# Optimization experiments

Measured on AMD Instinct MI355X. Metric: run time of the kernel, lower is better.

The kernel has to match this reference:

```python
import jax, jax.numpy as jnp
import numpy as np

B, T, C, H, E, K = 4, 2048, 512, 2048, 8, 2


def setup_inputs() -> dict:
    key = jax.random.key(0)
    ks = jax.random.split(key, 7)
    s_r = 1.0 / np.sqrt(C)
    s_h = 1.0 / np.sqrt(H)
    return {
        "x": jax.random.normal(ks[0], (B, T, C), dtype=jnp.float32),
        "Wr": jax.random.uniform(ks[1], (C, E), jnp.float32, -s_r, s_r),
        "br": jax.random.uniform(ks[2], (E,), jnp.float32, -s_r, s_r),
        "W1": jax.random.uniform(ks[3], (E, C, H), jnp.float32, -s_r, s_r),
        "b1": jax.random.uniform(ks[4], (E, H), jnp.float32, -s_r, s_r),
        "W2": jax.random.uniform(ks[5], (E, H, C), jnp.float32, -s_h, s_h),
        "b2": jax.random.uniform(ks[6], (E, C), jnp.float32, -s_h, s_h),
    }


def reference(x, Wr, br, W1, b1, W2, b2):
    # Router logits [B,T,E]
    logits = jnp.einsum("btc,ce->bte", x, Wr) + br
    topk_vals, topk_idx = jax.lax.top_k(logits, K)  # [B,T,K]
    scores = jax.nn.softmax(topk_vals, axis=-1)  # softmax over the K selected
    # Combine weights per expert: gate[b,t,e] = sum_k scores[b,t,k]*(idx==e)
    onehot = jax.nn.one_hot(topk_idx, E, dtype=x.dtype)  # [B,T,K,E]
    gate = jnp.einsum("btk,btke->bte", scores, onehot)  # [B,T,E]
    # Dense-masked expert MLPs (tokens not routed to e have gate==0)
    h = jax.nn.relu(jnp.einsum("btc,ech->bteh", x, W1) + b1)  # [B,T,E,H]
    y = jnp.einsum("bteh,ehc->btec", h, W2) + b2  # [B,T,E,C]
    out = jnp.einsum("btec,bte->btc", y, gate)  # weighted combine
    return logits, topk_idx, out
```

## Files before the change

kernel.cpp:

```cpp
#include <hip/hip_runtime.h>
#include <hip/hip_bf16.h>

#define NTOK 8192
#define NASN 16384
#define C_ 512
#define H_ 2048
#define E_ 8
#define RBC 2048

typedef __bf16 bf16x8 __attribute__((ext_vector_type(8)));
typedef float f32x4 __attribute__((ext_vector_type(4)));

#define WS_COUNTS 0
#define WS_OFFS   65536
#define WS_T1S    65792
#define WS_INFO   66048
#define WS_TOKL   (WS_INFO + NTOK*16)
#define WS_SLOTS  (WS_TOKL + NASN*4)
#define WS_XBF    (WS_SLOTS + NTOK*8)
#define WS_W1B    (WS_XBF + (size_t)NTOK*C_*2)
#define WS_W2B    (WS_W1B + (size_t)E_*H_*C_*2)
#define WS_HS     (WS_W2B + (size_t)E_*H_*C_*2)
#define WS_YS     WS_XBF

__device__ __forceinline__ unsigned int f2bf(float f) {
  __hip_bfloat16 h = __float2bfloat16(f);
  return (unsigned int)*(unsigned short*)&h;
}
__device__ __forceinline__ float bf2f(unsigned int u) {
  return __int_as_float((u & 0xffffu) << 16);
}

__device__ __forceinline__ void g2l16(const unsigned short* g, unsigned short* l) {
  __builtin_amdgcn_global_load_lds(
      (const __attribute__((address_space(1))) unsigned int*)g,
      (__attribute__((address_space(3))) unsigned int*)l, 16, 0, 0);
}

__device__ __forceinline__ void stage_decode(int L, int& brow, int& q) {
  int s = L >> 3, slot = L & 7;
  int v = slot ^ (s & 7);
  brow = 2*s + (v >> 2);
  q = v & 3;
}

__global__ __launch_bounds__(256) void k_fused(
    const float* __restrict__ x, const float* __restrict__ Wr,
    const float* __restrict__ br, float* __restrict__ out_logits,
    float* __restrict__ out_idx, int4* __restrict__ info,
    int* __restrict__ counts, unsigned short* __restrict__ Xbf,
    const float* __restrict__ W1, unsigned short* __restrict__ W1b,
    const float* __restrict__ W2, unsigned short* __restrict__ W2b)
{
  __shared__ float tileS[128][33];
  __shared__ int bc[8];
  int b = blockIdx.x;
  int tid = threadIdx.x;

  if (b < RBC) {
    if (tid < 8) bc[tid] = 0;
    __syncthreads();
    int t = b * 4 + (tid >> 6);
    int lane = tid & 63;
    const float4* xr = (const float4*)(x + (size_t)t * C_);
    float4 x0 = xr[lane*2], x1 = xr[lane*2+1];
    uint4 pk;
    pk.x = f2bf(x0.x) | (f2bf(x0.y) << 16);
    pk.y = f2bf(x0.z) | (f2bf(x0.w) << 16);
    pk.z = f2bf(x1.x) | (f2bf(x1.y) << 16);
    pk.w = f2bf(x1.z) | (f2bf(x1.w) << 16);
    *(uint4*)(Xbf + (size_t)t * C_ + lane*8) = pk;

    float xs[8] = {x0.x,x0.y,x0.z,x0.w,x1.x,x1.y,x1.z,x1.w};
    float acc[8] = {0,0,0,0,0,0,0,0};
    #pragma unroll
    for (int j = 0; j < 8; j++) {
      const float4* w = (const float4*)(Wr + (size_t)(lane*8+j) * E_);
      float4 w0 = w[0], w1 = w[1];
      float we[8] = {w0.x,w0.y,w0.z,w0.w,w1.x,w1.y,w1.z,w1.w};
      #pragma unroll
      for (int e = 0; e < 8; e++) acc[e] += xs[j] * we[e];
    }
    #pragma unroll
    for (int off = 1; off < 64; off <<= 1) {
      #pragma unroll
      for (int e = 0; e < 8; e++) acc[e] += __shfl_xor(acc[e], off, 64);
    }
    #pragma unroll
    for (int e = 0; e < 8; e++) acc[e] += br[e];
    if (lane == 0) {
      #pragma unroll
      for (int e = 0; e < 8; e++) out_logits[t*8 + e] = acc[e];
      int i0 = 0; float v0 = acc[0];
      #pragma unroll
      for (int e = 1; e < 8; e++) if (acc[e] > v0) { v0 = acc[e]; i0 = e; }
      int i1 = -1; float v1 = -1e30f;
      #pragma unroll
      for (int e = 0; e < 8; e++) if (e != i0 && acc[e] > v1) { v1 = acc[e]; i1 = e; }
      float d = expf(v1 - v0);
      float s1 = d / (1.0f + d);
      float s0 = 1.0f - s1;
      out_idx[t*2]     = (float)i0;
      out_idx[t*2 + 1] = (float)i1;
      info[t] = make_int4(i0, i1, __float_as_int(s0), __float_as_int(s1));
      atomicAdd(&bc[i0], 1);
      atomicAdd(&bc[i1], 1);
    }
    __syncthreads();
    if (tid < 8) counts[b*8 + tid] = bc[tid];
    return;
  }

  const float* in; unsigned short* outp; int R, S, bx, by, bz;
  if (b < 2*RBC) {
    int bb = b - RBC;
    in = W1; outp = W1b; R = C_; S = H_;
    bx = bb & 63; by = (bb >> 6) & 3; bz = bb >> 8;
  } else {
    int bb = b - 2*RBC;
    in = W2; outp = W2b; R = H_; S = C_;
    bx = bb & 15; by = (bb >> 4) & 15; bz = bb >> 8;
  }
  size_t zo = (size_t)bz * R * S;
  in += zo; outp += zo;
  int r0 = by * 128, s0 = bx * 32;
  #pragma unroll
  for (int i = 0; i < 16; i++) {
    int lin = i*256 + tid;
    int rr = lin >> 5, ss = lin & 31;
    tileS[rr][ss] = in[(size_t)(r0 + rr) * S + s0 + ss];
  }
  __syncthreads();
  #pragma unroll
  for (int i = 0; i < 4; i++) {
    int lin = i*256 + tid;
    int ss = lin >> 5, rq = lin & 31;
    ushort4 v;
    v.x = (unsigned short)f2bf(tileS[rq*4+0][ss]);
    v.y = (unsigned short)f2bf(tileS[rq*4+1][ss]);
    v.z = (unsigned short)f2bf(tileS[rq*4+2][ss]);
    v.w = (unsigned short)f2bf(tileS[rq*4+3][ss]);
    *(ushort4*)(outp + (size_t)(s0 + ss) * R + r0 + rq*4) = v;
  }
}

__global__ __launch_bounds__(64) void k_prefscatter(
    const int* __restrict__ counts, const int4* __restrict__ info,
    int* __restrict__ tokl, int2* __restrict__ slots2,
    int* __restrict__ offs, int* __restrict__ t1s)
{
  __shared__ int full_s[8][8];
  __shared__ int part_s[8][8];
  __shared__ int tot_s[8];
  __shared__ int off_s[9];
  __shared__ int cur[8];
  int c = blockIdx.x, t = threadIdx.x;
  int e = t & 7, g = t >> 3;
  int lim = c * 16;
  int full = 0, part = 0;
  for (int i = 0; i < 256; i++) {
    int rb = g*256 + i;
    int v = counts[rb*8 + e];
    full += v;
    if (rb < lim) part += v;
  }
  full_s[e][g] = full; part_s[e][g] = part;
  __syncthreads();
  if (t < 8) {
    int s = 0;
    #pragma unroll
    for (int gg = 0; gg < 8; gg++) s += full_s[t][gg];
    tot_s[t] = s;
  }
  __syncthreads();
  if (t == 0) {
    int o = 0;
    off_s[0] = 0;
    for (int ee = 0; ee < 8; ee++) { o += tot_s[ee]; off_s[ee+1] = o; }
    if (c == 0) {
      offs[0] = 0; t1s[0] = 0;
      int tt = 0;
      for (int ee = 0; ee < 8; ee++) {
        offs[ee+1] = off_s[ee+1];
        tt += (tot_s[ee] + 127) >> 7;
        t1s[ee+1] = tt;
      }
    }
  }
  __syncthreads();
  if (t < 8) {
    int mg = c >> 4;
    int bse = off_s[t];
    #pragma unroll
    for (int gg = 0; gg < 8; gg++) if (gg < mg) bse += full_s[t][gg];
    bse += part_s[t][mg];
    cur[t] = bse;
  }
  __syncthreads();
  int tok = c*64 + t;
  int4 nfo = info[tok];
  int r0 = atomicAdd(&cur[nfo.x], 1);
  int r1 = atomicAdd(&cur[nfo.y], 1);
  tokl[r0] = tok;
  tokl[r1] = tok;
  slots2[tok] = make_int2(r0, r1);
}

__global__ __launch_bounds__(512) void k_gemm1(
    const unsigned short* __restrict__ Xbf, const int* __restrict__ tokl,
    const unsigned short* __restrict__ W1b,
    const float* __restrict__ b1, unsigned short* __restrict__ Hs,
    const int* __restrict__ offs, const int* __restrict__ t1s)
{
  __shared__ __align__(16) unsigned short AB[2*8192];
  int b = blockIdx.x;
  int mo = b >> 7, rr = b & 127;
  int n0 = (rr >> 3) * 128;
  int mt = mo*8 + (rr & 7);
  if (mt >= t1s[8]) return;
  int e = 0;
  #pragma unroll
  for (int i = 0; i < 7; i++) if (mt >= t1s[e+1]) e++;
  int row0 = offs[e] + (mt - t1s[e]) * 128;
  int rowEnd = offs[e+1];
  int tid = threadIdx.x, lane = tid & 63, w = tid >> 6;
  int wm = (w >> 2) * 64, wn = (w & 3) * 32;
  int quad = lane >> 4, l16 = lane & 15;
  const f32x4 zero = {0.f, 0.f, 0.f, 0.f};
  f32x4 acc[4][2];
  #pragma unroll
  for (int i = 0; i < 4; i++)
    #pragma unroll
    for (int j = 0; j < 2; j++) acc[i][j] = zero;
  const unsigned short* Bsrc = W1b + ((size_t)e * H_ + n0) * C_;

  const unsigned short* ga; const unsigned short* gb;
  int lao, lbo;
  {
    int L = w*64 + lane;
    int brow, q; stage_decode(L, brow, q);
    int gr = row0 + brow; gr = gr < NASN-1 ? gr : NASN-1;
    int trow = tokl[gr];
    ga = Xbf + (size_t)trow * C_ + q*8;
    gb = Bsrc + (size_t)brow * C_ + q*8;
    lao = w*512;
    lbo = 4096 + w*512;
  }
  int rbase = (l16>>1)*64 + ((((l16&1)<<2) + quad) ^ (l16>>1))*8;
  const int KI = C_ / 32;

  g2l16(ga, AB + lao); g2l16(gb, AB + lbo);

  for (int ki = 0; ki < KI; ki++) {
    int p = ki & 1;
    if (ki + 1 < KI) {
      int off = (ki + 1) * 32;
      unsigned short* nb = AB + (p ^ 1) * 8192;
      g2l16(ga + off, nb + lao);
      g2l16(gb + off, nb + lbo);
      asm volatile("s_waitcnt vmcnt(2)" ::: "memory");
    } else {
      asm volatile("s_waitcnt vmcnt(0)" ::: "memory");
    }
    asm volatile("s_barrier" ::: "memory");

    const unsigned short* Ap = AB + p*8192;
    const unsigned short* Bp = Ap + 4096;
    bf16x8 af[4], bfr[2];
    #pragma unroll
    for (int i = 0; i < 4; i++)
      af[i] = *(const bf16x8*)&Ap[wm*32 + i*512 + rbase];
    #pragma unroll
    for (int j = 0; j < 2; j++)
      bfr[j] = *(const bf16x8*)&Bp[wn*32 + j*512 + rbase];
    #pragma unroll
    for (int i = 0; i < 4; i++)
      #pragma unroll
      for (int j = 0; j < 2; j++)
        acc[i][j] = __builtin_amdgcn_mfma_f32_16x16x32_bf16(af[i], bfr[j], acc[i][j], 0, 0, 0);

    asm volatile("s_waitcnt lgkmcnt(0)" ::: "memory");
    asm volatile("s_barrier" ::: "memory");
  }

  unsigned short* Lt = AB + w*2048;
  #pragma unroll
  for (int j = 0; j < 2; j++) {
    int n = n0 + wn + j*16 + l16;
    float bias = b1[e * H_ + n];
    #pragma unroll
    for (int i = 0; i < 4; i++)
      #pragma unroll
      for (int r = 0; r < 4; r++) {
        float v = acc[i][j][r] + bias;
        Lt[(i*16 + quad*4 + r)*32 + j*16 + l16] = (unsigned short)f2bf(v > 0.f ? v : 0.f);
      }
  }
  #pragma unroll
  for (int it = 0; it < 4; it++) {
    int rloc = it*16 + (lane >> 2);
    int m = row0 + wm + rloc;
    uint4 vv = *(uint4*)&Lt[rloc*32 + (lane & 3)*8];
    if (m < rowEnd)
      *(uint4*)(Hs + (size_t)m * H_ + n0 + wn + (lane & 3)*8) = vv;
  }
}

__global__ __launch_bounds__(512) void k_gemm2(
    const unsigned short* __restrict__ Hs, const unsigned short* __restrict__ W2b,
    const float* __restrict__ b2, unsigned short* __restrict__ Ys,
    const int* __restrict__ offs, const int* __restrict__ t1s)
{
  __shared__ __align__(16) unsigned short AB[2*8192];
  int b = blockIdx.x;
  int mo = b >> 5, rr = b & 31;
  int n0 = (rr >> 3) * 128;
  int mt = mo*8 + (rr & 7);
  if (mt >= t1s[8]) return;
  int e = 0;
  #pragma unroll
  for (int i = 0; i < 7; i++) if (mt >= t1s[e+1]) e++;
  int row0 = offs[e] + (mt - t1s[e]) * 128;
  int rowEnd = offs[e+1];
  int tid = threadIdx.x, lane = tid & 63, w = tid >> 6;
  int wm = (w >> 2) * 64, wn = (w & 3) * 32;
  int quad = lane >> 4, l16 = lane & 15;
  const f32x4 zero = {0.f, 0.f, 0.f, 0.f};
  f32x4 acc[4][2];
  #pragma unroll
  for (int i = 0; i < 4; i++)
    #pragma unroll
    for (int j = 0; j < 2; j++) acc[i][j] = zero;
  const unsigned short* Bsrc = W2b + ((size_t)e * C_ + n0) * H_;

  const unsigned short* ga; const unsigned short* gb;
  int lao, lbo;
  {
    int L = w*64 + lane;
    int brow, q; stage_decode(L, brow, q);
    int gr = row0 + brow; gr = gr < NASN-1 ? gr : NASN-1;
    ga = Hs + (size_t)gr * H_ + q*8;
    gb = Bsrc + (size_t)brow * H_ + q*8;
    lao = w*512;
    lbo = 4096 + w*512;
  }
  int rbase = (l16>>1)*64 + ((((l16&1)<<2) + quad) ^ (l16>>1))*8;
  const int KI = H_ / 32;

  g2l16(ga, AB + lao); g2l16(gb, AB + lbo);

  for (int ki = 0; ki < KI; ki++) {
    int p = ki & 1;
    if (ki + 1 < KI) {
      int off = (ki + 1) * 32;
      unsigned short* nb = AB + (p ^ 1) * 8192;
      g2l16(ga + off, nb + lao);
      g2l16(gb + off, nb + lbo);
      asm volatile("s_waitcnt vmcnt(2)" ::: "memory");
    } else {
      asm volatile("s_waitcnt vmcnt(0)" ::: "memory");
    }
    asm volatile("s_barrier" ::: "memory");

    const unsigned short* Ap = AB + p*8192;
    const unsigned short* Bp = Ap + 4096;
    bf16x8 af[4], bfr[2];
    #pragma unroll
    for (int i = 0; i < 4; i++)
      af[i] = *(const bf16x8*)&Ap[wm*32 + i*512 + rbase];
    #pragma unroll
    for (int j = 0; j < 2; j++)
      bfr[j] = *(const bf16x8*)&Bp[wn*32 + j*512 + rbase];
    #pragma unroll
    for (int i = 0; i < 4; i++)
      #pragma unroll
      for (int j = 0; j < 2; j++)
        acc[i][j] = __builtin_amdgcn_mfma_f32_16x16x32_bf16(af[i], bfr[j], acc[i][j], 0, 0, 0);

    asm volatile("s_waitcnt lgkmcnt(0)" ::: "memory");
    asm volatile("s_barrier" ::: "memory");
  }

  unsigned short* Lt = AB + w*2048;
  #pragma unroll
  for (int j = 0; j < 2; j++) {
    int n = n0 + wn + j*16 + l16;
    float bias = b2[e * C_ + n];
    #pragma unroll
    for (int i = 0; i < 4; i++)
      #pragma unroll
      for (int r = 0; r < 4; r++)
        Lt[(i*16 + quad*4 + r)*32 + j*16 + l16] =
            (unsigned short)f2bf(acc[i][j][r] + bias);
  }
  #pragma unroll
  for (int it = 0; it < 4; it++) {
    int rloc = it*16 + (lane >> 2);
    int m = row0 + wm + rloc;
    uint4 vv = *(uint4*)&Lt[rloc*32 + (lane & 3)*8];
    if (m < rowEnd)
      *(uint4*)(Ys + (size_t)m * C_ + n0 + wn + (lane & 3)*8) = vv;
  }
}

__global__ __launch_bounds__(256) void k_combine(
    const unsigned short* __restrict__ Ys, const int4* __restrict__ info,
    const int2* __restrict__ slots2, float* __restrict__ outp)
{
  int t = blockIdx.x * 4 + (threadIdx.x >> 6);
  int lane = threadIdx.x & 63;
  int4 nfo = info[t];
  int2 ss = slots2[t];
  float g0 = __int_as_float(nfo.z), g1 = __int_as_float(nfo.w);
  uint4 a = *(const uint4*)(Ys + (size_t)ss.x * C_ + lane*8);
  uint4 bb = *(const uint4*)(Ys + (size_t)ss.y * C_ + lane*8);
  unsigned int au[4] = {a.x, a.y, a.z, a.w};
  unsigned int bu[4] = {bb.x, bb.y, bb.z, bb.w};
  float vals[8];
  #pragma unroll
  for (int q = 0; q < 4; q++) {
    vals[q*2]   = g0*bf2f(au[q])       + g1*bf2f(bu[q]);
    vals[q*2+1] = g0*bf2f(au[q] >> 16) + g1*bf2f(bu[q] >> 16);
  }
  float4 o0, o1;
  o0.x = vals[0]; o0.y = vals[1]; o0.z = vals[2]; o0.w = vals[3];
  o1.x = vals[4]; o1.y = vals[5]; o1.z = vals[6]; o1.w = vals[7];
  float4* o = (float4*)(outp + (size_t)t * C_ + lane*8);
  o[0] = o0;
  o[1] = o1;
}

extern "C" void kernel_launch(void* const* d_in, const int* in_sizes, int n_in,
                              void* d_out, int out_size, void* d_ws, size_t ws_size,
                              hipStream_t stream)
{
  const float* x  = (const float*)d_in[0];
  const float* Wr = (const float*)d_in[1];
  const float* br = (const float*)d_in[2];
  const float* W1 = (const float*)d_in[3];
  const float* b1 = (const float*)d_in[4];
  const float* W2 = (const float*)d_in[5];
  const float* b2 = (const float*)d_in[6];
  float* out = (float*)d_out;
  char* ws = (char*)d_ws;

  int*  counts = (int*)(ws + WS_COUNTS);
  int*  offs   = (int*)(ws + WS_OFFS);
  int*  t1s    = (int*)(ws + WS_T1S);
  int4* info   = (int4*)(ws + WS_INFO);
  int*  tokl   = (int*)(ws + WS_TOKL);
  int2* slots2 = (int2*)(ws + WS_SLOTS);
  unsigned short* Xbf = (unsigned short*)(ws + WS_XBF);
  unsigned short* W1b = (unsigned short*)(ws + WS_W1B);
  unsigned short* W2b = (unsigned short*)(ws + WS_W2B);
  unsigned short* Hs  = (unsigned short*)(ws + WS_HS);
  unsigned short* Ys  = (unsigned short*)(ws + WS_YS);

  k_fused<<<3*RBC, 256, 0, stream>>>(x, Wr, br, out, out + 65536, info,
                                     counts, Xbf, W1, W1b, W2, W2b);
  k_prefscatter<<<128, 64, 0, stream>>>(counts, info, tokl, slots2, offs, t1s);
  k_gemm1<<<17*128, 512, 0, stream>>>(Xbf, tokl, W1b, b1, Hs, offs, t1s);
  k_gemm2<<<17*32, 512, 0, stream>>>(Hs, W2b, b2, Ys, offs, t1s);
  k_combine<<<NTOK/4, 256, 0, stream>>>(Ys, info, slots2, out + 81920);
}
```

Baseline: 270.1 us.

## Triple-buffer LDS in expert GEMMs with one barrier per K step

Both grouped GEMM kernels now use three LDS stages instead of two and prefetch two K-tiles ahead. The second barrier per iteration is dropped, because the stage being overwritten was last read two iterations earlier. Fragment loads are split into two halves with MFMA bursts between them under raised wave priority (s_setprio). This aims to hide global-load latency and barrier stalls, at the cost of 48KB of LDS per block, which may lower occupancy.

```diff
diff --git a/kernel.cpp b/kernel.cpp
--- a/kernel.cpp
+++ b/kernel.cpp
@@ -206,13 +206,54 @@
   slots2[tok] = make_int2(r0, r1);
 }
 
+#define KLOOP(KI)                                                              \
+  {                                                                            \
+    int cOff = 0, sOff = 2*8192;                                               \
+    for (int ki = 0; ki < (KI); ki++) {                                        \
+      if (ki + 1 < (KI))                                                       \
+        asm volatile("s_waitcnt vmcnt(2)" ::: "memory");                       \
+      else                                                                     \
+        asm volatile("s_waitcnt vmcnt(0)" ::: "memory");                       \
+      asm volatile("s_barrier" ::: "memory");                                  \
+      if (ki + 2 < (KI)) {                                                     \
+        int off_ = (ki + 2) * 32;                                              \
+        unsigned short* nb_ = AB + sOff;                                       \
+        g2l16(ga + off_, nb_ + lao);                                           \
+        g2l16(gb + off_, nb_ + lbo);                                           \
+      }                                                                        \
+      const unsigned short* Ap_ = AB + cOff;                                   \
+      const unsigned short* Bp_ = Ap_ + 4096;                                  \
+      bf16x8 af0 = *(const bf16x8*)&Ap_[wm*32 + 0*512 + rbase];                \
+      bf16x8 af1 = *(const bf16x8*)&Ap_[wm*32 + 1*512 + rbase];                \
+      bf16x8 bf0 = *(const bf16x8*)&Bp_[wn*32 + 0*512 + rbase];                \
+      bf16x8 bf1 = *(const bf16x8*)&Bp_[wn*32 + 1*512 + rbase];                \
+      __builtin_amdgcn_s_setprio(1);                                           \
+      acc[0][0] = __builtin_amdgcn_mfma_f32_16x16x32_bf16(af0, bf0, acc[0][0], 0, 0, 0); \
+      acc[0][1] = __builtin_amdgcn_mfma_f32_16x16x32_bf16(af0, bf1, acc[0][1], 0, 0, 0); \
+      acc[1][0] = __builtin_amdgcn_mfma_f32_16x16x32_bf16(af1, bf0, acc[1][0], 0, 0, 0); \
+      acc[1][1] = __builtin_amdgcn_mfma_f32_16x16x32_bf16(af1, bf1, acc[1][1], 0, 0, 0); \
+      __builtin_amdgcn_s_setprio(0);                                           \
+      bf16x8 af2 = *(const bf16x8*)&Ap_[wm*32 + 2*512 + rbase];                \
+      bf16x8 af3 = *(const bf16x8*)&Ap_[wm*32 + 3*512 + rbase];                \
+      __builtin_amdgcn_s_setprio(1);                                           \
+      acc[2][0] = __builtin_amdgcn_mfma_f32_16x16x32_bf16(af2, bf0, acc[2][0], 0, 0, 0); \
+      acc[2][1] = __builtin_amdgcn_mfma_f32_16x16x32_bf16(af2, bf1, acc[2][1], 0, 0, 0); \
+      acc[3][0] = __builtin_amdgcn_mfma_f32_16x16x32_bf16(af3, bf0, acc[3][0], 0, 0, 0); \
+      acc[3][1] = __builtin_amdgcn_mfma_f32_16x16x32_bf16(af3, bf1, acc[3][1], 0, 0, 0); \
+      __builtin_amdgcn_s_setprio(0);                                           \
+      asm volatile("s_waitcnt lgkmcnt(0)" ::: "memory");                       \
+      cOff += 8192; if (cOff == 3*8192) cOff = 0;                              \
+      sOff += 8192; if (sOff == 3*8192) sOff = 0;                              \
+    }                                                                          \
+  }
+
 __global__ __launch_bounds__(512) void k_gemm1(
     const unsigned short* __restrict__ Xbf, const int* __restrict__ tokl,
     const unsigned short* __restrict__ W1b,
     const float* __restrict__ b1, unsigned short* __restrict__ Hs,
     const int* __restrict__ offs, const int* __restrict__ t1s)
 {
-  __shared__ __align__(16) unsigned short AB[2*8192];
+  __shared__ __align__(16) unsigned short AB[3*8192];
   int b = blockIdx.x;
   int mo = b >> 7, rr = b & 127;
   int n0 = (rr >> 3) * 128;
@@ -249,39 +290,10 @@
   int rbase = (l16>>1)*64 + ((((l16&1)<<2) + quad) ^ (l16>>1))*8;
   const int KI = C_ / 32;
 
-  g2l16(ga, AB + lao); g2l16(gb, AB + lbo);
-
-  for (int ki = 0; ki < KI; ki++) {
-    int p = ki & 1;
-    if (ki + 1 < KI) {
-      int off = (ki + 1) * 32;
-      unsigned short* nb = AB + (p ^ 1) * 8192;
-      g2l16(ga + off, nb + lao);
-      g2l16(gb + off, nb + lbo);
-      asm volatile("s_waitcnt vmcnt(2)" ::: "memory");
-    } else {
-      asm volatile("s_waitcnt vmcnt(0)" ::: "memory");
-    }
-    asm volatile("s_barrier" ::: "memory");
-
-    const unsigned short* Ap = AB + p*8192;
-    const unsigned short* Bp = Ap + 4096;
-    bf16x8 af[4], bfr[2];
-    #pragma unroll
-    for (int i = 0; i < 4; i++)
-      af[i] = *(const bf16x8*)&Ap[wm*32 + i*512 + rbase];
-    #pragma unroll
-    for (int j = 0; j < 2; j++)
-      bfr[j] = *(const bf16x8*)&Bp[wn*32 + j*512 + rbase];
-    #pragma unroll
-    for (int i = 0; i < 4; i++)
-      #pragma unroll
-      for (int j = 0; j < 2; j++)
-        acc[i][j] = __builtin_amdgcn_mfma_f32_16x16x32_bf16(af[i], bfr[j], acc[i][j], 0, 0, 0);
-
-    asm volatile("s_waitcnt lgkmcnt(0)" ::: "memory");
-    asm volatile("s_barrier" ::: "memory");
-  }
+  g2l16(ga, AB + lao);            g2l16(gb, AB + lbo);
+  g2l16(ga + 32, AB + 8192 + lao); g2l16(gb + 32, AB + 8192 + lbo);
+
+  KLOOP(KI);
 
   unsigned short* Lt = AB + w*2048;
   #pragma unroll
@@ -311,7 +323,7 @@
     const float* __restrict__ b2, unsigned short* __restrict__ Ys,
     const int* __restrict__ offs, const int* __restrict__ t1s)
 {
-  __shared__ __align__(16) unsigned short AB[2*8192];
+  __shared__ __align__(16) unsigned short AB[3*8192];
   int b = blockIdx.x;
   int mo = b >> 5, rr = b & 31;
   int n0 = (rr >> 3) * 128;
@@ -347,39 +359,10 @@
   int rbase = (l16>>1)*64 + ((((l16&1)<<2) + quad) ^ (l16>>1))*8;
   const int KI = H_ / 32;
 
-  g2l16(ga, AB + lao); g2l16(gb, AB + lbo);
-
-  for (int ki = 0; ki < KI; ki++) {
-    int p = ki & 1;
-    if (ki + 1 < KI) {
-      int off = (ki + 1) * 32;
-      unsigned short* nb = AB + (p ^ 1) * 8192;
-      g2l16(ga + off, nb + lao);
-      g2l16(gb + off, nb + lbo);
-      asm volatile("s_waitcnt vmcnt(2)" ::: "memory");
-    } else {
-      asm volatile("s_waitcnt vmcnt(0)" ::: "memory");
-    }
-    asm volatile("s_barrier" ::: "memory");
-
-    const unsigned short* Ap = AB + p*8192;
-    const unsigned short* Bp = Ap + 4096;
-    bf16x8 af[4], bfr[2];
-    #pragma unroll
-    for (int i = 0; i < 4; i++)
-      af[i] = *(const bf16x8*)&Ap[wm*32 + i*512 + rbase];
-    #pragma unroll
-    for (int j = 0; j < 2; j++)
-      bfr[j] = *(const bf16x8*)&Bp[wn*32 + j*512 + rbase];
-    #pragma unroll
-    for (int i = 0; i < 4; i++)
-      #pragma unroll
-      for (int j = 0; j < 2; j++)
-        acc[i][j] = __builtin_amdgcn_mfma_f32_16x16x32_bf16(af[i], bfr[j], acc[i][j], 0, 0, 0);
-
-    asm volatile("s_waitcnt lgkmcnt(0)" ::: "memory");
-    asm volatile("s_barrier" ::: "memory");
-  }
+  g2l16(ga, AB + lao);            g2l16(gb, AB + lbo);
+  g2l16(ga + 32, AB + 8192 + lao); g2l16(gb + 32, AB + 8192 + lbo);
+
+  KLOOP(KI);
 
   unsigned short* Lt = AB + w*2048;
   #pragma unroll
```

Measured after the change: 266.8 us. About the same (-1.2%).
